# Kernel optimization log

Measured on AMD Instinct MI355X. Metric: run time of the kernel, lower is better.

## Reference

```python
import jax, jax.numpy as jnp
import numpy as np

N_NODES = 50000
IN_CH = 128
HID = 128
N_EDGES = 800000


def _glorot(key, shape):
    fan_in, fan_out = shape[0], shape[1]
    lim = (6.0 / (fan_in + fan_out)) ** 0.5
    return jax.random.uniform(key, shape, jnp.float32, -lim, lim)


def setup_inputs() -> dict:
    key = jax.random.key(0)
    ks = jax.random.split(key, 8)
    x = jax.random.normal(ks[0], (N_NODES, IN_CH), jnp.float32)
    edge_index = jax.random.randint(ks[1], (2, N_EDGES), 0, N_NODES, jnp.int64)
    return {
        "x": x,
        "edge_index": edge_index,
        # SAGEConv1: lin_l (with bias) applied to mean-aggregated neighbors,
        # lin_r (no bias) applied to root features (PyG defaults, mean aggr)
        "W1l": _glorot(ks[2], (IN_CH, HID)),
        "b1l": jnp.zeros((HID,), jnp.float32),
        "W1r": _glorot(ks[3], (IN_CH, HID)),
        # SAGEConv2
        "W2l": _glorot(ks[4], (HID, HID)),
        "b2l": jnp.zeros((HID,), jnp.float32),
        "W2r": _glorot(ks[5], (HID, HID)),
        # final Linear(hidden, 1)
        "Wout": _glorot(ks[6], (HID, 1)),
        "bout": jnp.zeros((1,), jnp.float32),
    }


def _sage_conv(x, src, dst, Wl, bl, Wr, n_nodes):
    # gather source features along edges, mean-reduce into destinations
    msgs = x[src]                                                # [E, D]
    sums = jax.ops.segment_sum(msgs, dst, num_segments=n_nodes)  # [N, D]
    cnt = jax.ops.segment_sum(jnp.ones((src.shape[0], 1), x.dtype), dst,
                              num_segments=n_nodes)              # [N, 1]
    agg = sums / jnp.maximum(cnt, 1.0)
    return agg @ Wl + bl + x @ Wr


def reference(x, edge_index, W1l, b1l, W1r, W2l, b2l, W2r, Wout, bout):
    src, dst = edge_index[0], edge_index[1]
    n = x.shape[0]
    h = jax.nn.relu(_sage_conv(x, src, dst, W1l, b1l, W1r, n))
    h = jax.nn.relu(_sage_conv(h, src, dst, W2l, b2l, W2r, n))
    return (h @ Wout + bout).squeeze(-1)  # [N]
```

## Files before the change

kernel.cpp:

```cpp
#include <hip/hip_runtime.h>

#define D 128
#define LSTR 132
#define HB 256
#define SCAN_NPB 4096

typedef __attribute__((ext_vector_type(8))) short short8;
typedef __attribute__((ext_vector_type(4))) float f32x4;

static __device__ __forceinline__ unsigned short f2bf(float f) {
    unsigned u = __float_as_uint(f);
    return (unsigned short)((u + 0x7fffu + ((u >> 16) & 1u)) >> 16);
}
static __device__ __forceinline__ float b2f(unsigned short u) {
    return __uint_as_float(((unsigned)u) << 16);
}


__global__ __launch_bounds__(256) void prep_hist_kernel(
    const float* __restrict__ x, const float* __restrict__ W1l,
    const float* __restrict__ W1r, const float* __restrict__ W2l,
    const float* __restrict__ W2r, unsigned* __restrict__ xb2,
    unsigned short* __restrict__ Bt1, unsigned short* __restrict__ Bt2,
    int NX2, const int* __restrict__ dst, int E, int* __restrict__ deg) {
    const int t = threadIdx.x;
    if (blockIdx.x < HB) {
        const int per = (E + HB - 1) / HB;
        const int lo = blockIdx.x * per;
        const int hi = min(lo + per, E);
        for (int i = lo + t; i < hi; i += 256) atomicAdd(&deg[dst[i]], 1);
        return;
    }
    const int i = (blockIdx.x - HB) * 256 + t;
    if (i < NX2) {
        const float2 v = *(const float2*)(x + 2 * (size_t)i);
        xb2[i] = (unsigned)f2bf(v.x) | ((unsigned)f2bf(v.y) << 16);
    } else if (i < NX2 + 2 * 32768) {
        const int j = i - NX2;
        const int which = j >> 15;
        const int jj = j & 32767;
        const int n = jj >> 8;
        const int k = jj & 255;
        const float* Wl = which ? W2l : W1l;
        const float* Wr = which ? W2r : W1r;
        const float w = (k < 128) ? Wl[k * 128 + n] : Wr[(k - 128) * 128 + n];
        (which ? Bt2 : Bt1)[jj] = f2bf(w);
    }
}

__global__ __launch_bounds__(256) void scan1_kernel(const int* __restrict__ deg,
                                                    int N,
                                                    int* __restrict__ bsum) {
    const int t = threadIdx.x;
    const int lo = blockIdx.x * SCAN_NPB + t * 16;
    int s = 0;
    if (lo + 16 <= N) {
        const int4* p = (const int4*)(deg + lo);
#pragma unroll
        for (int i = 0; i < 4; ++i) {
            const int4 v = p[i];
            s += v.x + v.y + v.z + v.w;
        }
    } else {
        for (int i = lo; i < min(lo + 16, N); ++i) s += deg[i];
    }
#pragma unroll
    for (int off = 1; off < 64; off <<= 1) s += __shfl_xor(s, off, 64);
    __shared__ int ws[4];
    if ((t & 63) == 0) ws[t >> 6] = s;
    __syncthreads();
    if (t == 0) bsum[blockIdx.x] = ws[0] + ws[1] + ws[2] + ws[3];
}

__global__ __launch_bounds__(256) void scan2_kernel(
    const int* __restrict__ deg, int N, int E, int nbins,
    const int* __restrict__ bsum, int* __restrict__ cursor,
    int* __restrict__ tile_base, float* __restrict__ invL_g) {
    __shared__ int ws[5];
    const int t = threadIdx.x;
    const int b = blockIdx.x;
    if (t == 0) {
        int base = 0;
        for (int i = 0; i < b; ++i) base += bsum[i];
        ws[4] = base;
    }
    const int lo = b * SCAN_NPB + t * 16;
    int d[16];
    int s = 0;
    if (lo + 16 <= N) {
        const int4* p = (const int4*)(deg + lo);
#pragma unroll
        for (int i = 0; i < 4; ++i) {
            const int4 v = p[i];
            d[4 * i + 0] = v.x;
            d[4 * i + 1] = v.y;
            d[4 * i + 2] = v.z;
            d[4 * i + 3] = v.w;
            s += v.x + v.y + v.z + v.w;
        }
    } else {
#pragma unroll
        for (int i = 0; i < 16; ++i) {
            d[i] = (lo + i < N) ? deg[lo + i] : 0;
            s += d[i];
        }
    }
    int sc = s;
#pragma unroll
    for (int off = 1; off < 64; off <<= 1) {
        const int u = __shfl_up(sc, off, 64);
        if ((t & 63) >= off) sc += u;
    }
    if ((t & 63) == 63) ws[t >> 6] = sc;
    __syncthreads();
    int run = ws[4] + sc - s;
    for (int w = 0; w < (t >> 6); ++w) run += ws[w];
#pragma unroll
    for (int i = 0; i < 16; ++i) {
        const int idx = lo + i;
        if (idx < N) {
            cursor[idx] = run;
            if ((idx & 31) == 0) tile_base[idx >> 5] = run;
            invL_g[idx] = 1.0f / fmaxf((float)d[i], 1.0f);
            run += d[i];
        }
    }
    if (b == 0 && t == 0) tile_base[nbins] = E;
}

__global__ __launch_bounds__(256) void fill_kernel(
    const int* __restrict__ src, const int* __restrict__ dst, int E,
    int* __restrict__ cursor, unsigned* __restrict__ csr) {
    const int i = blockIdx.x * 256 + threadIdx.x;
    if (i < E) {
        const int d = dst[i];
        const int pos = atomicAdd(&cursor[d], 1);
        csr[pos] = (unsigned)src[i] | ((unsigned)d << 16);
    }
}

template <bool HEAD, int GV>
__global__ __launch_bounds__(256) void sage_kernel(
    const unsigned short* __restrict__ xb, const unsigned* __restrict__ csr,
    const int* __restrict__ tile_base, const float* __restrict__ invL_g,
    const unsigned short* __restrict__ Bt,
    const float* __restrict__ bl, const float* __restrict__ Wout,
    const float* __restrict__ bout, unsigned short* __restrict__ hb_out,
    float* __restrict__ out, int N) {
    __shared__ float aggL[32 * LSTR];
    __shared__ float invL[32];
    __shared__ float redH[64];

    const int b = blockIdx.x;
    const int i0 = b * 32;
    const int t = threadIdx.x;
    const int g = t >> 5;
    const int l = t & 31;
    const int c4 = l << 2;

    for (int i = t; i < 32 * LSTR; i += 256) aggL[i] = 0.f;
    if (t < 32) invL[t] = (i0 + t < N) ? invL_g[i0 + t] : 1.0f;
    __syncthreads();

    const int rs0 = tile_base[b];
    const int re0 = tile_base[b + 1];
    const int nE = re0 - rs0;
    int e = rs0 + ((nE * g) >> 3);
    const int ee = rs0 + ((nE * (g + 1)) >> 3);

    float4 acc = make_float4(0.f, 0.f, 0.f, 0.f);

    if (GV == 0) {
        int cur = (e < ee) ? (int)(csr[e] >> 16) - i0 : -1;
        auto load4 = [&](unsigned p) -> float4 {
            const ushort4 u =
                *(const ushort4*)(xb + (size_t)(p & 0xffffu) * D + c4);
            float4 v;
            v.x = b2f(u.x); v.y = b2f(u.y); v.z = b2f(u.z); v.w = b2f(u.w);
            return v;
        };
        auto step = [&](unsigned p, const float4& v) {
            const int r = (int)(p >> 16) - i0;
            if (r != cur) {
                float* q = aggL + cur * LSTR + c4;
                atomicAdd(q + 0, acc.x);
                atomicAdd(q + 1, acc.y);
                atomicAdd(q + 2, acc.z);
                atomicAdd(q + 3, acc.w);
                acc = make_float4(0.f, 0.f, 0.f, 0.f);
                cur = r;
            }
            acc.x += v.x; acc.y += v.y; acc.z += v.z; acc.w += v.w;
        };
        while (e + 8 <= ee) {
            const unsigned p0 = csr[e + 0], p1 = csr[e + 1];
            const unsigned p2 = csr[e + 2], p3 = csr[e + 3];
            const unsigned p4 = csr[e + 4], p5 = csr[e + 5];
            const unsigned p6 = csr[e + 6], p7 = csr[e + 7];
            const float4 v0 = load4(p0), v1 = load4(p1), v2 = load4(p2),
                         v3 = load4(p3), v4 = load4(p4), v5 = load4(p5),
                         v6 = load4(p6), v7 = load4(p7);
            step(p0, v0); step(p1, v1); step(p2, v2); step(p3, v3);
            step(p4, v4); step(p5, v5); step(p6, v6); step(p7, v7);
            e += 8;
        }
        while (e < ee) {
            const unsigned p = csr[e];
            step(p, load4(p));
            ++e;
        }
        if (cur >= 0) {
            float* q = aggL + cur * LSTR + c4;
            atomicAdd(q + 0, acc.x);
            atomicAdd(q + 1, acc.y);
            atomicAdd(q + 2, acc.z);
            atomicAdd(q + 3, acc.w);
        }
    } else {
        int cur = -1;
        auto flush = [&]() {
            float* q = aggL + cur * LSTR + c4;
            atomicAdd(q + 0, acc.x);
            atomicAdd(q + 1, acc.y);
            atomicAdd(q + 2, acc.z);
            atomicAdd(q + 3, acc.w);
        };
        auto step = [&](unsigned p, uint2 u) {
            const int r = (int)(p >> 16) - i0;
            if (r != cur) {
                if (cur >= 0) flush();
                acc = make_float4(0.f, 0.f, 0.f, 0.f);
                cur = r;
            }
            acc.x += __uint_as_float(u.x << 16);
            acc.y += __uint_as_float(u.x & 0xffff0000u);
            acc.z += __uint_as_float(u.y << 16);
            acc.w += __uint_as_float(u.y & 0xffff0000u);
        };
        const int e0 = e;
        const int nfull = (ee - e) >> 3;
        unsigned pc[8];
        if (nfull > 0) {
#pragma unroll
            for (int i = 0; i < 8; ++i) pc[i] = csr[e + i];
        }
        for (int k = 0; k < nfull; ++k) {
            uint2 u[8];
#pragma unroll
            for (int i = 0; i < 8; ++i)
                u[i] = *(const uint2*)(xb + (size_t)(pc[i] & 0xffffu) * D + c4);
            unsigned pf[8];
            if (k + 1 < nfull) {
#pragma unroll
                for (int i = 0; i < 8; ++i) pf[i] = csr[e + 8 + i];
            }
#pragma unroll
            for (int i = 0; i < 8; ++i) step(pc[i], u[i]);
            if (k + 1 < nfull) {
#pragma unroll
                for (int i = 0; i < 8; ++i) pc[i] = pf[i];
            }
            e += 8;
        }
        for (e = e0 + nfull * 8; e < ee; ++e) {
            const unsigned p = csr[e];
            const uint2 u =
                *(const uint2*)(xb + (size_t)(p & 0xffffu) * D + c4);
            step(p, u);
        }
        if (cur >= 0) flush();
    }
    __syncthreads();

    const int wave = t >> 6;
    const int lane = t & 63;
    const int ln = lane & 15;
    const int quad = lane >> 4;
    const int mtile = wave & 1;
    const int nt0 = (wave >> 1) * 4;
    const int mrow = mtile * 16 + ln;
    const int gmr = i0 + mrow;
    const float inv = invL[mrow];

    f32x4 acc4[4] = {f32x4{0.f, 0.f, 0.f, 0.f}, f32x4{0.f, 0.f, 0.f, 0.f},
                     f32x4{0.f, 0.f, 0.f, 0.f}, f32x4{0.f, 0.f, 0.f, 0.f}};

#pragma unroll
    for (int s = 0; s < 4; ++s) {
        const int kb = s * 32 + quad * 8;
        const float* ap = aggL + mrow * LSTR + kb;
        const float4 fa = *(const float4*)ap;
        const float4 fb = *(const float4*)(ap + 4);
        const short8 aA = {(short)f2bf(fa.x * inv), (short)f2bf(fa.y * inv),
                           (short)f2bf(fa.z * inv), (short)f2bf(fa.w * inv),
                           (short)f2bf(fb.x * inv), (short)f2bf(fb.y * inv),
                           (short)f2bf(fb.z * inv), (short)f2bf(fb.w * inv)};
        short8 aX = {0, 0, 0, 0, 0, 0, 0, 0};
        if (gmr < N) aX = *(const short8*)(xb + (size_t)gmr * D + kb);
#pragma unroll
        for (int nt = 0; nt < 4; ++nt) {
            const int n = (nt0 + nt) * 16 + ln;
            const short8 b1 = *(const short8*)(Bt + n * 256 + kb);
            const short8 b2 = *(const short8*)(Bt + n * 256 + 128 + kb);
            acc4[nt] = __builtin_amdgcn_mfma_f32_16x16x32_bf16(aA, b1, acc4[nt],
                                                               0, 0, 0);
            acc4[nt] = __builtin_amdgcn_mfma_f32_16x16x32_bf16(aX, b2, acc4[nt],
                                                               0, 0, 0);
        }
    }

    float biasv[4], woutv[4];
#pragma unroll
    for (int nt = 0; nt < 4; ++nt) {
        const int col = (nt0 + nt) * 16 + ln;
        biasv[nt] = bl[col];
        if (HEAD) woutv[nt] = Wout[col];
    }

    if (!HEAD) {
#pragma unroll
        for (int r = 0; r < 4; ++r) {
            const int gr = i0 + mtile * 16 + quad * 4 + r;
            if (gr < N) {
#pragma unroll
                for (int nt = 0; nt < 4; ++nt) {
                    const int col = (nt0 + nt) * 16 + ln;
                    const float v = fmaxf(acc4[nt][r] + biasv[nt], 0.f);
                    hb_out[(size_t)gr * D + col] = f2bf(v);
                }
            }
        }
    } else {
        const float b0 = bout[0];
#pragma unroll
        for (int r = 0; r < 4; ++r) {
            const int row = mtile * 16 + quad * 4 + r;
            float p = 0.f;
#pragma unroll
            for (int nt = 0; nt < 4; ++nt) {
                const float v = fmaxf(acc4[nt][r] + biasv[nt], 0.f);
                p += v * woutv[nt];
            }
            p += __shfl_xor(p, 1);
            p += __shfl_xor(p, 2);
            p += __shfl_xor(p, 4);
            p += __shfl_xor(p, 8);
            if (ln == 0) redH[row * 2 + (wave >> 1)] = p;
        }
        __syncthreads();
        if (t < 32) {
            const int gr = i0 + t;
            if (gr < N) out[gr] = redH[t * 2] + redH[t * 2 + 1] + b0;
        }
    }
}

extern "C" void kernel_launch(void* const* d_in, const int* in_sizes, int n_in,
                              void* d_out, int out_size, void* d_ws,
                              size_t ws_size, hipStream_t stream) {
    const float* x = (const float*)d_in[0];
    const int* ei = (const int*)d_in[1];
    const float* W1l = (const float*)d_in[2];
    const float* b1l = (const float*)d_in[3];
    const float* W1r = (const float*)d_in[4];
    const float* W2l = (const float*)d_in[5];
    const float* b2l = (const float*)d_in[6];
    const float* W2r = (const float*)d_in[7];
    const float* Wout = (const float*)d_in[8];
    const float* bout = (const float*)d_in[9];

    const int N = in_sizes[0] / D;
    const int E = in_sizes[1] / 2;
    const int* src = ei;
    const int* dst = ei + E;

    const int nbins = (N + 31) / 32;
    const size_t Npad = (size_t)((N + 255) & ~255);
    const size_t Epad = (size_t)((E + 255) & ~255);

    int* deg = (int*)d_ws;
    int* cursor = deg + Npad;
    int* tile_base = cursor + Npad;
    int* bsum = tile_base + 2052;
    float* invL_g = (float*)(bsum + 64);
    unsigned* csr = (unsigned*)(invL_g + Npad);
    unsigned short* xb = (unsigned short*)(csr + Epad);
    unsigned short* hb = xb + (size_t)N * D;
    unsigned short* Bt1 = hb + (size_t)N * D;
    unsigned short* Bt2 = Bt1 + 128 * 256;
    float* out = (float*)d_out;

    const int NX2 = N * D / 2;
    const int prep_blocks = (NX2 + 2 * 32768 + 255) / 256;
    const int nsb = (N + SCAN_NPB - 1) / SCAN_NPB;

    hipMemsetAsync(deg, 0, Npad * sizeof(int), stream);
    prep_hist_kernel<<<HB + prep_blocks, 256, 0, stream>>>(
        x, W1l, W1r, W2l, W2r, (unsigned*)xb, Bt1, Bt2, NX2, dst, E, deg);
    scan1_kernel<<<nsb, 256, 0, stream>>>(deg, N, bsum);
    scan2_kernel<<<nsb, 256, 0, stream>>>(deg, N, E, nbins, bsum, cursor,
                                          tile_base, invL_g);
    fill_kernel<<<(E + 255) / 256, 256, 0, stream>>>(src, dst, E, cursor, csr);

    sage_kernel<false, 0><<<nbins, 256, 0, stream>>>(
        xb, csr, tile_base, invL_g, Bt1, b1l, nullptr, nullptr, hb, nullptr, N);
    sage_kernel<true, 1><<<nbins, 256, 0, stream>>>(
        hb, csr, tile_base, invL_g, Bt2, b2l, Wout, bout, nullptr, out, N);
}
```

Measured before the change: 308.4 us.

## Stage neighbor gathers into LDS via async global_load_lds triple buffering

The edge-gather aggregation now has each wave stream 8 neighbor rows per step straight into a triple-buffered LDS stage using global_load_lds. It overlaps the gather latency with the accumulation through explicit vmcnt waits. Work is split per wave (4 ranges) rather than per 32-lane group (8), and each lane owns 2 columns. The prep kernel also converts x to bf16 four elements per thread. The LDS footprint and the reliance on hand-written waitcnt ordering are the added risk.

New measurement: 398.4 us. 1.29x slower.

```diff
diff --git a/kernel.cpp b/kernel.cpp
--- a/kernel.cpp
+++ b/kernel.cpp
@@ -4,6 +4,7 @@
 #define LSTR 132
 #define HB 256
 #define SCAN_NPB 4096
+#define NBUF 3
 
 typedef __attribute__((ext_vector_type(8))) short short8;
 typedef __attribute__((ext_vector_type(4))) float f32x4;
@@ -12,17 +13,21 @@
     unsigned u = __float_as_uint(f);
     return (unsigned short)((u + 0x7fffu + ((u >> 16) & 1u)) >> 16);
 }
-static __device__ __forceinline__ float b2f(unsigned short u) {
-    return __uint_as_float(((unsigned)u) << 16);
+
+static __device__ __forceinline__ void gload_lds16(const unsigned short* g,
+                                                   unsigned* l) {
+    __builtin_amdgcn_global_load_lds(
+        (const __attribute__((address_space(1))) void*)g,
+        (__attribute__((address_space(3))) void*)l, 16, 0, 0);
 }
 
 
 __global__ __launch_bounds__(256) void prep_hist_kernel(
     const float* __restrict__ x, const float* __restrict__ W1l,
     const float* __restrict__ W1r, const float* __restrict__ W2l,
-    const float* __restrict__ W2r, unsigned* __restrict__ xb2,
+    const float* __restrict__ W2r, uint2* __restrict__ xb4,
     unsigned short* __restrict__ Bt1, unsigned short* __restrict__ Bt2,
-    int NX2, const int* __restrict__ dst, int E, int* __restrict__ deg) {
+    int NX4, const int* __restrict__ dst, int E, int* __restrict__ deg) {
     const int t = threadIdx.x;
     if (blockIdx.x < HB) {
         const int per = (E + HB - 1) / HB;
@@ -32,11 +37,14 @@
         return;
     }
     const int i = (blockIdx.x - HB) * 256 + t;
-    if (i < NX2) {
-        const float2 v = *(const float2*)(x + 2 * (size_t)i);
-        xb2[i] = (unsigned)f2bf(v.x) | ((unsigned)f2bf(v.y) << 16);
-    } else if (i < NX2 + 2 * 32768) {
-        const int j = i - NX2;
+    if (i < NX4) {
+        const float4 v = *(const float4*)(x + 4 * (size_t)i);
+        uint2 o;
+        o.x = (unsigned)f2bf(v.x) | ((unsigned)f2bf(v.y) << 16);
+        o.y = (unsigned)f2bf(v.z) | ((unsigned)f2bf(v.w) << 16);
+        xb4[i] = o;
+    } else if (i < NX4 + 2 * 32768) {
+        const int j = i - NX4;
         const int which = j >> 15;
         const int jj = j & 32767;
         const int n = jj >> 8;
@@ -139,7 +147,7 @@
     }
 }
 
-template <bool HEAD, int GV>
+template <bool HEAD>
 __global__ __launch_bounds__(256) void sage_kernel(
     const unsigned short* __restrict__ xb, const unsigned* __restrict__ csr,
     const int* __restrict__ tile_base, const float* __restrict__ invL_g,
@@ -148,15 +156,18 @@
     const float* __restrict__ bout, unsigned short* __restrict__ hb_out,
     float* __restrict__ out, int N) {
     __shared__ float aggL[32 * LSTR];
+    __shared__ __align__(16) unsigned stageB[4][NBUF][8][64];
+    __shared__ int rowid[4][NBUF][8];
     __shared__ float invL[32];
     __shared__ float redH[64];
 
     const int b = blockIdx.x;
     const int i0 = b * 32;
     const int t = threadIdx.x;
-    const int g = t >> 5;
-    const int l = t & 31;
-    const int c4 = l << 2;
+    const int wv = t >> 6;
+    const int lane = t & 63;
+    const int sub = lane >> 4;
+    const int cl = lane & 15;
 
     for (int i = t; i < 32 * LSTR; i += 256) aggL[i] = 0.f;
     if (t < 32) invL[t] = (i0 + t < N) ? invL_g[i0 + t] : 1.0f;
@@ -165,119 +176,85 @@
     const int rs0 = tile_base[b];
     const int re0 = tile_base[b + 1];
     const int nE = re0 - rs0;
-    int e = rs0 + ((nE * g) >> 3);
-    const int ee = rs0 + ((nE * (g + 1)) >> 3);
-
-    float4 acc = make_float4(0.f, 0.f, 0.f, 0.f);
-
-    if (GV == 0) {
-        int cur = (e < ee) ? (int)(csr[e] >> 16) - i0 : -1;
-        auto load4 = [&](unsigned p) -> float4 {
-            const ushort4 u =
-                *(const ushort4*)(xb + (size_t)(p & 0xffffu) * D + c4);
-            float4 v;
-            v.x = b2f(u.x); v.y = b2f(u.y); v.z = b2f(u.z); v.w = b2f(u.w);
-            return v;
-        };
-        auto step = [&](unsigned p, const float4& v) {
-            const int r = (int)(p >> 16) - i0;
-            if (r != cur) {
-                float* q = aggL + cur * LSTR + c4;
-                atomicAdd(q + 0, acc.x);
-                atomicAdd(q + 1, acc.y);
-                atomicAdd(q + 2, acc.z);
-                atomicAdd(q + 3, acc.w);
-                acc = make_float4(0.f, 0.f, 0.f, 0.f);
-                cur = r;
+    const int ws = rs0 + ((nE * wv) >> 2);
+    const int we = rs0 + ((nE * (wv + 1)) >> 2);
+    const int cnt = we - ws;
+    const int nb = (cnt + 7) >> 3;
+    const int lastc = re0 - 1;
+
+    auto ldcs = [&](int s, unsigned& A, unsigned& B_) {
+        const int e0 = ws + s * 8;
+        A = csr[min(e0 + sub, lastc)];
+        B_ = csr[min(e0 + 4 + sub, lastc)];
+    };
+    auto issue = [&](int s, unsigned A, unsigned B_) {
+        unsigned* lp = &stageB[wv][s % NBUF][0][0];
+        const unsigned short* gA = xb + (size_t)(A & 0xffffu) * D + cl * 8;
+        const unsigned short* gB = xb + (size_t)(B_ & 0xffffu) * D + cl * 8;
+        gload_lds16(gA, lp);
+        gload_lds16(gB, lp + 256);
+        if (cl == 0) {
+            rowid[wv][s % NBUF][sub] = (int)(A >> 16);
+            rowid[wv][s % NBUF][4 + sub] = (int)(B_ >> 16);
+        }
+    };
+
+    float a0 = 0.f, a1 = 0.f;
+    int cur = -1;
+    if (nb > 0) {
+        unsigned cA0, cB0, cA1, cB1, cA2 = 0, cB2 = 0;
+        ldcs(0, cA0, cB0);
+        if (nb > 1) ldcs(1, cA1, cB1);
+        if (nb > 2) ldcs(2, cA2, cB2);
+        issue(0, cA0, cB0);
+        if (nb > 1) issue(1, cA1, cB1);
+        for (int k = 0; k < nb; ++k) {
+            if (k + 2 < nb) {
+                unsigned nA = 0, nB = 0;
+                if (k + 3 < nb) ldcs(k + 3, nA, nB);
+                issue(k + 2, cA2, cB2);
+                cA2 = nA;
+                cB2 = nB;
+            } else if (k + 1 < nb) {
+                asm volatile("s_waitcnt vmcnt(2)" ::: "memory");
+            } else {
+                asm volatile("s_waitcnt vmcnt(0)" ::: "memory");
             }
-            acc.x += v.x; acc.y += v.y; acc.z += v.z; acc.w += v.w;
-        };
-        while (e + 8 <= ee) {
-            const unsigned p0 = csr[e + 0], p1 = csr[e + 1];
-            const unsigned p2 = csr[e + 2], p3 = csr[e + 3];
-            const unsigned p4 = csr[e + 4], p5 = csr[e + 5];
-            const unsigned p6 = csr[e + 6], p7 = csr[e + 7];
-            const float4 v0 = load4(p0), v1 = load4(p1), v2 = load4(p2),
-                         v3 = load4(p3), v4 = load4(p4), v5 = load4(p5),
-                         v6 = load4(p6), v7 = load4(p7);
-            step(p0, v0); step(p1, v1); step(p2, v2); step(p3, v3);
-            step(p4, v4); step(p5, v5); step(p6, v6); step(p7, v7);
-            e += 8;
-        }
-        while (e < ee) {
-            const unsigned p = csr[e];
-            step(p, load4(p));
-            ++e;
+            __builtin_amdgcn_sched_barrier(0);
+            const unsigned* sb = &stageB[wv][k % NBUF][0][0];
+            const int* rd = &rowid[wv][k % NBUF][0];
+            const int c = min(8, cnt - k * 8);
+#pragma unroll
+            for (int i = 0; i < 8; ++i) {
+                if (i < c) {
+                    const int r = rd[i] - i0;
+                    const unsigned u = sb[i * 64 + lane];
+                    if (r != cur) {
+                        if (cur >= 0) {
+                            atomicAdd(&aggL[cur * LSTR + 2 * lane], a0);
+                            atomicAdd(&aggL[cur * LSTR + 2 * lane + 1], a1);
+                        }
+                        a0 = 0.f;
+                        a1 = 0.f;
+                        cur = r;
+                    }
+                    a0 += __uint_as_float(u << 16);
+                    a1 += __uint_as_float(u & 0xffff0000u);
+                }
+            }
+            __builtin_amdgcn_sched_barrier(0);
         }
         if (cur >= 0) {
-            float* q = aggL + cur * LSTR + c4;
-            atomicAdd(q + 0, acc.x);
-            atomicAdd(q + 1, acc.y);
-            atomicAdd(q + 2, acc.z);
-            atomicAdd(q + 3, acc.w);
-        }
-    } else {
-        int cur = -1;
-        auto flush = [&]() {
-            float* q = aggL + cur * LSTR + c4;
-            atomicAdd(q + 0, acc.x);
-            atomicAdd(q + 1, acc.y);
-            atomicAdd(q + 2, acc.z);
-            atomicAdd(q + 3, acc.w);
-        };
-        auto step = [&](unsigned p, uint2 u) {
-            const int r = (int)(p >> 16) - i0;
-            if (r != cur) {
-                if (cur >= 0) flush();
-                acc = make_float4(0.f, 0.f, 0.f, 0.f);
-                cur = r;
-            }
-            acc.x += __uint_as_float(u.x << 16);
-            acc.y += __uint_as_float(u.x & 0xffff0000u);
-            acc.z += __uint_as_float(u.y << 16);
-            acc.w += __uint_as_float(u.y & 0xffff0000u);
-        };
-        const int e0 = e;
-        const int nfull = (ee - e) >> 3;
-        unsigned pc[8];
-        if (nfull > 0) {
-#pragma unroll
-            for (int i = 0; i < 8; ++i) pc[i] = csr[e + i];
-        }
-        for (int k = 0; k < nfull; ++k) {
-            uint2 u[8];
-#pragma unroll
-            for (int i = 0; i < 8; ++i)
-                u[i] = *(const uint2*)(xb + (size_t)(pc[i] & 0xffffu) * D + c4);
-            unsigned pf[8];
-            if (k + 1 < nfull) {
-#pragma unroll
-                for (int i = 0; i < 8; ++i) pf[i] = csr[e + 8 + i];
-            }
-#pragma unroll
-            for (int i = 0; i < 8; ++i) step(pc[i], u[i]);
-            if (k + 1 < nfull) {
-#pragma unroll
-                for (int i = 0; i < 8; ++i) pc[i] = pf[i];
-            }
-            e += 8;
-        }
-        for (e = e0 + nfull * 8; e < ee; ++e) {
-            const unsigned p = csr[e];
-            const uint2 u =
-                *(const uint2*)(xb + (size_t)(p & 0xffffu) * D + c4);
-            step(p, u);
-        }
-        if (cur >= 0) flush();
+            atomicAdd(&aggL[cur * LSTR + 2 * lane], a0);
+            atomicAdd(&aggL[cur * LSTR + 2 * lane + 1], a1);
+        }
     }
     __syncthreads();
 
-    const int wave = t >> 6;
-    const int lane = t & 63;
     const int ln = lane & 15;
     const int quad = lane >> 4;
-    const int mtile = wave & 1;
-    const int nt0 = (wave >> 1) * 4;
+    const int mtile = wv & 1;
+    const int nt0 = (wv >> 1) * 4;
     const int mrow = mtile * 16 + ln;
     const int gmr = i0 + mrow;
     const float inv = invL[mrow];
@@ -345,7 +322,7 @@
             p += __shfl_xor(p, 2);
             p += __shfl_xor(p, 4);
             p += __shfl_xor(p, 8);
-            if (ln == 0) redH[row * 2 + (wave >> 1)] = p;
+            if (ln == 0) redH[row * 2 + (wv >> 1)] = p;
         }
         __syncthreads();
         if (t < 32) {
@@ -390,20 +367,20 @@
     unsigned short* Bt2 = Bt1 + 128 * 256;
     float* out = (float*)d_out;
 
-    const int NX2 = N * D / 2;
-    const int prep_blocks = (NX2 + 2 * 32768 + 255) / 256;
+    const int NX4 = N * D / 4;
+    const int prep_blocks = (NX4 + 2 * 32768 + 255) / 256;
     const int nsb = (N + SCAN_NPB - 1) / SCAN_NPB;
 
     hipMemsetAsync(deg, 0, Npad * sizeof(int), stream);
     prep_hist_kernel<<<HB + prep_blocks, 256, 0, stream>>>(
-        x, W1l, W1r, W2l, W2r, (unsigned*)xb, Bt1, Bt2, NX2, dst, E, deg);
+        x, W1l, W1r, W2l, W2r, (uint2*)xb, Bt1, Bt2, NX4, dst, E, deg);
     scan1_kernel<<<nsb, 256, 0, stream>>>(deg, N, bsum);
     scan2_kernel<<<nsb, 256, 0, stream>>>(deg, N, E, nbins, bsum, cursor,
                                           tile_base, invL_g);
     fill_kernel<<<(E + 255) / 256, 256, 0, stream>>>(src, dst, E, cursor, csr);
 
-    sage_kernel<false, 0><<<nbins, 256, 0, stream>>>(
+    sage_kernel<false><<<nbins, 256, 0, stream>>>(
         xb, csr, tile_base, invL_g, Bt1, b1l, nullptr, nullptr, hb, nullptr, N);
-    sage_kernel<true, 1><<<nbins, 256, 0, stream>>>(
+    sage_kernel<true><<<nbins, 256, 0, stream>>>(
         hb, csr, tile_base, invL_g, Bt2, b2l, Wout, bout, nullptr, out, N);
 }
```
